# Kernel tuning notes

Measured on AMD Instinct MI355X. Metric: run time of the kernel, lower is better.

## Reference

```python
import jax, jax.numpy as jnp
import numpy as np
import math

ANSWER_LEN = 11; D_MODEL = 6; FFN_DIM = 3; HEAD_DIM = 3; MAX_SEQ_LEN = 34
N_HEADS = 2; POS_DIM = 3; TOK_DIM = 3; VOCAB_SIZE = 14; MAX_DIGITS = 10
EOS_TOKEN = 12; EQUALS_TOKEN = 11; PAD_TOKEN = 13; PLUS_TOKEN = 10
B, T = 65536, 34


def _spiral(i, period):
    return (math.cos(2 * math.pi * i / period), math.sin(2 * math.pi * i / period), i / max(period - 1, 1))


def _build_pos_enc():
    N_POS = 10
    pe = np.zeros((MAX_SEQ_LEN, POS_DIM), dtype=np.float32)
    for i in range(MAX_DIGITS):
        pe[i] = _spiral(i, N_POS)
    for i in range(MAX_DIGITS):
        pe[11 + i] = _spiral(i, N_POS)
    for i in range(min(ANSWER_LEN, N_POS)):
        pe[22 + i] = _spiral(i, N_POS)
    pe[32] = [0.0, 0.0, 1.5]
    pe[10] = [2.0, 0.0, -1.0]
    pe[21] = [0.0, 2.0, -1.0]
    pe[33] = [-2.0, 0.0, -1.0]
    return pe


def _build_tok_emb():
    emb = np.zeros((VOCAB_SIZE, TOK_DIM), dtype=np.float32)
    for d in range(10):
        emb[d] = _spiral(d, 10)
    emb[PLUS_TOKEN] = [2.0, 0.0, -1.0]
    emb[EQUALS_TOKEN] = [0.0, 2.0, -1.0]
    emb[EOS_TOKEN] = [-2.0, 0.0, -1.0]
    emb[PAD_TOKEN] = [0.0, -2.0, -1.0]
    return emb


def setup_inputs() -> dict:
    key = jax.random.key(0)
    ks = jax.random.split(key, 12)
    H = N_HEADS * HEAD_DIM  # 6

    def lin(k, out_d, in_d):
        bound = 1.0 / math.sqrt(in_d)
        return jax.random.uniform(k, (out_d, in_d), jnp.float32, -bound, bound)

    return {
        'idx': jax.random.randint(ks[0], (B, T), 0, VOCAB_SIZE),
        'tok_emb': jnp.asarray(_build_tok_emb()),
        'pos_enc': jnp.asarray(_build_pos_enc()),
        'q_w': lin(ks[1], H, POS_DIM),
        'k_w': lin(ks[2], H, POS_DIM),
        'v_w': lin(ks[3], H, TOK_DIM),
        'out_w': lin(ks[4], D_MODEL, H),
        'ln1_g': jnp.ones((D_MODEL,)), 'ln1_b': jnp.zeros((D_MODEL,)),
        'ln2_g': jnp.ones((D_MODEL,)), 'ln2_b': jnp.zeros((D_MODEL,)),
        'lnf_g': jnp.ones((D_MODEL,)), 'lnf_b': jnp.zeros((D_MODEL,)),
        'ffn_w1': lin(ks[5], FFN_DIM, D_MODEL),
        'ffn_b1': jax.random.uniform(ks[6], (FFN_DIM,), jnp.float32, -1/math.sqrt(D_MODEL), 1/math.sqrt(D_MODEL)),
        'ffn_w2': lin(ks[7], D_MODEL, FFN_DIM),
        'ffn_b2': jax.random.uniform(ks[8], (D_MODEL,), jnp.float32, -1/math.sqrt(FFN_DIM), 1/math.sqrt(FFN_DIM)),
        'head_w': lin(ks[9], TOK_DIM, D_MODEL),
    }


def _ln(x, g, b, eps=1e-5):
    mu = jnp.mean(x, -1, keepdims=True)
    var = jnp.mean((x - mu) ** 2, -1, keepdims=True)
    return (x - mu) * jax.lax.rsqrt(var + eps) * g + b


def reference(idx, tok_emb, pos_enc, q_w, k_w, v_w, out_w,
              ln1_g, ln1_b, ln2_g, ln2_b, lnf_g, lnf_b,
              ffn_w1, ffn_b1, ffn_w2, ffn_b2, head_w):
    b, t = idx.shape
    tok = tok_emb[idx]                              # [B,T,3]
    pos = jnp.broadcast_to(pos_enc[:t][None], (b, t, POS_DIM))
    x = jnp.concatenate([tok, pos], -1)             # [B,T,6]
    h = _ln(x, ln1_g, ln1_b)
    x_tok, x_pos = h[..., :TOK_DIM], h[..., TOK_DIM:]
    q = (x_pos @ q_w.T).reshape(b, t, N_HEADS, HEAD_DIM)
    k = (x_pos @ k_w.T).reshape(b, t, N_HEADS, HEAD_DIM)
    v = (x_tok @ v_w.T).reshape(b, t, N_HEADS, HEAD_DIM)
    attn = jnp.einsum('bqhd,bkhd->bhqk', q, k) / math.sqrt(HEAD_DIM)
    mask = jnp.tril(jnp.ones((t, t), dtype=bool))
    attn = jnp.where(mask[None, None], attn, -jnp.inf)
    attn = jax.nn.softmax(attn, -1)
    out = jnp.einsum('bhqk,bkhd->bqhd', attn, v).reshape(b, t, N_HEADS * HEAD_DIM)
    x = x + out @ out_w.T
    h2 = _ln(x, ln2_g, ln2_b)
    ffn = jax.nn.gelu(h2 @ ffn_w1.T + ffn_b1, approximate=False) @ ffn_w2.T + ffn_b2
    x = x + ffn
    x = _ln(x, lnf_g, lnf_b)
    return (x @ head_w.T) @ tok_emb.T               # [B,T,VOCAB]
```

## Files before the change

### kernel.cpp

```cpp
#include <hip/hip_runtime.h>
#include <math.h>

#define TT  34
#define VV  14
#define BLK 256


__global__ __launch_bounds__(BLK) void addtx_fwd(
    const int*   __restrict__ idx,
    const float* __restrict__ tok_emb,
    const float* __restrict__ pos_enc,
    const float* __restrict__ q_w,
    const float* __restrict__ k_w,
    const float* __restrict__ v_w,
    const float* __restrict__ out_w,
    const float* __restrict__ ln1_g, const float* __restrict__ ln1_b,
    const float* __restrict__ ln2_g, const float* __restrict__ ln2_b,
    const float* __restrict__ lnf_g, const float* __restrict__ lnf_b,
    const float* __restrict__ ffn_w1, const float* __restrict__ ffn_b1,
    const float* __restrict__ ffn_w2, const float* __restrict__ ffn_b2,
    const float* __restrict__ head_w,
    float* __restrict__ out)
{
    __shared__ float4 kvtab[TT * VV * 3];
    __shared__ float  wsm[192];
    __shared__ float  lgs[BLK * VV];

    const int tid = threadIdx.x;
    const int blk = blockIdx.x;

    {
        const int i = tid;
        if (i < 36)       wsm[i] = out_w[i];
        else if (i < 42)  wsm[i] = ln2_g[i - 36];
        else if (i < 48)  wsm[i] = ln2_b[i - 42];
        else if (i < 66)  wsm[i] = ffn_w1[i - 48];
        else if (i < 69)  wsm[i] = ffn_b1[i - 66];
        else if (i < 87)  wsm[i] = ffn_w2[i - 69];
        else if (i < 93)  wsm[i] = ffn_b2[i - 87];
        else if (i < 99)  wsm[i] = lnf_g[i - 93];
        else if (i < 105) wsm[i] = lnf_b[i - 99];
        else if (i < 189) {
            const int j = i - 105, v = j / 6, d = j - v * 6;
            wsm[i] = head_w[0 * 6 + d] * tok_emb[v * 3 + 0]
                   + head_w[1 * 6 + d] * tok_emb[v * 3 + 1]
                   + head_w[2 * 6 + d] * tok_emb[v * 3 + 2];
        }
    }

    const float rs3 = 0.57735026918962576f;
    for (int e = tid; e < TT * VV; e += BLK) {
        const int pos = e / VV, id = e - pos * VV;
        float x[6];
        x[0] = tok_emb[id * 3 + 0]; x[1] = tok_emb[id * 3 + 1]; x[2] = tok_emb[id * 3 + 2];
        x[3] = pos_enc[pos * 3 + 0]; x[4] = pos_enc[pos * 3 + 1]; x[5] = pos_enc[pos * 3 + 2];
        float mu = (x[0] + x[1] + x[2] + x[3] + x[4] + x[5]) * (1.0f / 6.0f);
        float var = 0.0f;
        #pragma unroll
        for (int d = 0; d < 6; ++d) { float dd = x[d] - mu; var += dd * dd; }
        const float rstd = rsqrtf(var * (1.0f / 6.0f) + 1e-5f);
        float h[6];
        #pragma unroll
        for (int d = 0; d < 6; ++d) h[d] = (x[d] - mu) * rstd * ln1_g[d] + ln1_b[d];
        float kk[6], vvv[6];
        #pragma unroll
        for (int r = 0; r < 6; ++r) {
            kk[r]  = (h[3] * k_w[r * 3 + 0] + h[4] * k_w[r * 3 + 1] + h[5] * k_w[r * 3 + 2]) * rs3;
            vvv[r] =  h[0] * v_w[r * 3 + 0] + h[1] * v_w[r * 3 + 1] + h[2] * v_w[r * 3 + 2];
        }
        kvtab[e * 3 + 0] = make_float4(kk[0], kk[1], kk[2], kk[3]);
        kvtab[e * 3 + 1] = make_float4(kk[4], kk[5], vvv[0], vvv[1]);
        kvtab[e * 3 + 2] = make_float4(vvv[2], vvv[3], vvv[4], vvv[5]);
    }
    __syncthreads();

    const int srank = (tid + ((blk & 3) << 6)) & (BLK - 1);
    const int r0 = (blk * BLK) % TT;
    int rem = srank, dsel = 0, ksel = 0, found = 0;
    #pragma unroll 1
    for (int tau = 0; tau < TT; ++tau) {
        int dlt = tau - r0; if (dlt < 0) dlt += TT;
        const int c = (dlt < (BLK % TT)) ? (BLK / TT + 1) : (BLK / TT);
        if (!found) {
            if (rem < c) { dsel = dlt; ksel = rem; found = 1; }
            else rem -= c;
        }
    }
    const int il   = dsel + ksel * TT;
    const int flat = blk * BLK + il;
    const int b    = flat / TT;
    const int t    = flat - b * TT;
    const int* __restrict__ row = idx + b * TT;

    float x[6];
    {
        const int mid = row[t];
        x[0] = tok_emb[mid * 3 + 0]; x[1] = tok_emb[mid * 3 + 1]; x[2] = tok_emb[mid * 3 + 2];
        x[3] = pos_enc[t * 3 + 0];   x[4] = pos_enc[t * 3 + 1];   x[5] = pos_enc[t * 3 + 2];
    }
    float q[6];
    {
        float mu = (x[0] + x[1] + x[2] + x[3] + x[4] + x[5]) * (1.0f / 6.0f);
        float var = 0.0f;
        #pragma unroll
        for (int d = 0; d < 6; ++d) { float dd = x[d] - mu; var += dd * dd; }
        const float rstd = rsqrtf(var * (1.0f / 6.0f) + 1e-5f);
        float h[6];
        #pragma unroll
        for (int d = 0; d < 6; ++d) h[d] = (x[d] - mu) * rstd * ln1_g[d] + ln1_b[d];
        #pragma unroll
        for (int r = 0; r < 6; ++r)
            q[r] = h[3] * q_w[r * 3 + 0] + h[4] * q_w[r * 3 + 1] + h[5] * q_w[r * 3 + 2];
    }

    float l0 = 0.f, l1 = 0.f;
    float a0 = 0.f, a1 = 0.f, a2 = 0.f, a3 = 0.f, a4 = 0.f, a5 = 0.f;
    int ebase = 0;
    for (int s = 0; s <= t; ++s) {
        const int ids = row[s];
        const float4* e4 = &kvtab[(ebase + ids) * 3];
        const float4 ka = e4[0];
        const float4 kb = e4[1];
        const float4 vb = e4[2];
        const float sc0 = q[0] * ka.x + q[1] * ka.y + q[2] * ka.z;
        const float sc1 = q[3] * ka.w + q[4] * kb.x + q[5] * kb.y;
        const float p0 = __expf(sc0);
        const float p1 = __expf(sc1);
        l0 += p0; l1 += p1;
        a0 += p0 * kb.z; a1 += p0 * kb.w; a2 += p0 * vb.x;
        a3 += p1 * vb.y; a4 += p1 * vb.z; a5 += p1 * vb.w;
        ebase += VV;
    }
    const float i0 = 1.0f / l0, i1 = 1.0f / l1;
    const float o6[6] = { a0 * i0, a1 * i0, a2 * i0, a3 * i1, a4 * i1, a5 * i1 };

    #pragma unroll
    for (int d = 0; d < 6; ++d) {
        float s = x[d];
        #pragma unroll
        for (int j = 0; j < 6; ++j) s += o6[j] * wsm[d * 6 + j];
        x[d] = s;
    }

    {
        float mu = (x[0] + x[1] + x[2] + x[3] + x[4] + x[5]) * (1.0f / 6.0f);
        float var = 0.0f;
        #pragma unroll
        for (int d = 0; d < 6; ++d) { float dd = x[d] - mu; var += dd * dd; }
        const float rstd = rsqrtf(var * (1.0f / 6.0f) + 1e-5f);
        float h2[6];
        #pragma unroll
        for (int d = 0; d < 6; ++d) h2[d] = (x[d] - mu) * rstd * wsm[36 + d] + wsm[42 + d];
        float g3[3];
        #pragma unroll
        for (int i = 0; i < 3; ++i) {
            float f = wsm[66 + i];
            #pragma unroll
            for (int d = 0; d < 6; ++d) f += h2[d] * wsm[48 + i * 6 + d];
            g3[i] = 0.5f * f * (1.0f + erff(f * 0.70710678118654752f));
        }
        #pragma unroll
        for (int d = 0; d < 6; ++d) {
            float s = x[d] + wsm[87 + d];
            #pragma unroll
            for (int i = 0; i < 3; ++i) s += g3[i] * wsm[69 + d * 3 + i];
            x[d] = s;
        }
    }

    {
        float mu = (x[0] + x[1] + x[2] + x[3] + x[4] + x[5]) * (1.0f / 6.0f);
        float var = 0.0f;
        #pragma unroll
        for (int d = 0; d < 6; ++d) { float dd = x[d] - mu; var += dd * dd; }
        const float rstd = rsqrtf(var * (1.0f / 6.0f) + 1e-5f);
        float xf[6];
        #pragma unroll
        for (int d = 0; d < 6; ++d) xf[d] = (x[d] - mu) * rstd * wsm[93 + d] + wsm[99 + d];
        #pragma unroll
        for (int v = 0; v < VV; ++v) {
            float s = 0.0f;
            #pragma unroll
            for (int d = 0; d < 6; ++d) s += xf[d] * wsm[105 + v * 6 + d];
            lgs[il * VV + v] = s;
        }
    }
    __syncthreads();

    float* __restrict__ ob = out + (size_t)blk * (BLK * VV);
    #pragma unroll
    for (int j = 0; j < VV; ++j)
        ob[j * BLK + tid] = lgs[j * BLK + tid];
}

extern "C" void kernel_launch(void* const* d_in, const int* in_sizes, int n_in,
                              void* d_out, int out_size, void* d_ws, size_t ws_size,
                              hipStream_t stream) {
    const int*   idx     = (const int*)  d_in[0];
    const float* tok_emb = (const float*)d_in[1];
    const float* pos_enc = (const float*)d_in[2];
    const float* q_w     = (const float*)d_in[3];
    const float* k_w     = (const float*)d_in[4];
    const float* v_w     = (const float*)d_in[5];
    const float* out_w   = (const float*)d_in[6];
    const float* ln1_g   = (const float*)d_in[7];
    const float* ln1_b   = (const float*)d_in[8];
    const float* ln2_g   = (const float*)d_in[9];
    const float* ln2_b   = (const float*)d_in[10];
    const float* lnf_g   = (const float*)d_in[11];
    const float* lnf_b   = (const float*)d_in[12];
    const float* ffn_w1  = (const float*)d_in[13];
    const float* ffn_b1  = (const float*)d_in[14];
    const float* ffn_w2  = (const float*)d_in[15];
    const float* ffn_b2  = (const float*)d_in[16];
    const float* head_w  = (const float*)d_in[17];
    float* out = (float*)d_out;

    const int n = in_sizes[0];
    const int blocks = n / BLK;
    addtx_fwd<<<blocks, BLK, 0, stream>>>(idx, tok_emb, pos_enc, q_w, k_w, v_w, out_w,
                                          ln1_g, ln1_b, ln2_g, ln2_b, lnf_g, lnf_b,
                                          ffn_w1, ffn_b1, ffn_w2, ffn_b2, head_w, out);
}
```

Baseline: 254.9 us.

## Stage token ids and embeddings in LDS, reuse KV table for output staging

```diff
diff --git a/kernel.cpp b/kernel.cpp
--- a/kernel.cpp
+++ b/kernel.cpp
@@ -4,6 +4,12 @@
 #define TT  34
 #define VV  14
 #define BLK 256
+
+#if __has_builtin(__builtin_amdgcn_exp2f)
+#define EXP2F(x) __builtin_amdgcn_exp2f(x)
+#else
+#define EXP2F(x) exp2f(x)
+#endif
 
 
 __global__ __launch_bounds__(BLK) void addtx_fwd(
@@ -22,9 +28,9 @@
     const float* __restrict__ head_w,
     float* __restrict__ out)
 {
-    __shared__ float4 kvtab[TT * VV * 3];
-    __shared__ float  wsm[192];
-    __shared__ float  lgs[BLK * VV];
+    __shared__ float4 kvs[TT * VV * 3];
+    __shared__ float  wsm[336];
+    __shared__ int    idsb[308];
 
     const int tid = threadIdx.x;
     const int blk = blockIdx.x;
@@ -46,9 +52,23 @@
                    + head_w[1 * 6 + d] * tok_emb[v * 3 + 1]
                    + head_w[2 * 6 + d] * tok_emb[v * 3 + 2];
         }
-    }
-
-    const float rs3 = 0.57735026918962576f;
+        if (tid < 144) {
+            const int k2 = 192 + tid;
+            wsm[k2] = (k2 < 234) ? tok_emb[k2 - 192] : pos_enc[k2 - 234];
+        }
+    }
+
+    const int ntot = (int)gridDim.x * BLK;
+    const int b0   = (blk * BLK) / TT;
+    {
+        const int gb = b0 * TT;
+        for (int e = tid; e < 308; e += BLK) {
+            const int g = gb + e;
+            idsb[e] = (g < ntot) ? idx[g] : 0;
+        }
+    }
+
+    const float rs3l = 0.57735026918962576f * 1.4426950408889634f;
     for (int e = tid; e < TT * VV; e += BLK) {
         const int pos = e / VV, id = e - pos * VV;
         float x[6];
@@ -65,38 +85,41 @@
         float kk[6], vvv[6];
         #pragma unroll
         for (int r = 0; r < 6; ++r) {
-            kk[r]  = (h[3] * k_w[r * 3 + 0] + h[4] * k_w[r * 3 + 1] + h[5] * k_w[r * 3 + 2]) * rs3;
+            kk[r]  = (h[3] * k_w[r * 3 + 0] + h[4] * k_w[r * 3 + 1] + h[5] * k_w[r * 3 + 2]) * rs3l;
             vvv[r] =  h[0] * v_w[r * 3 + 0] + h[1] * v_w[r * 3 + 1] + h[2] * v_w[r * 3 + 2];
         }
-        kvtab[e * 3 + 0] = make_float4(kk[0], kk[1], kk[2], kk[3]);
-        kvtab[e * 3 + 1] = make_float4(kk[4], kk[5], vvv[0], vvv[1]);
-        kvtab[e * 3 + 2] = make_float4(vvv[2], vvv[3], vvv[4], vvv[5]);
+        kvs[e * 3 + 0] = make_float4(kk[0], kk[1], kk[2], kk[3]);
+        kvs[e * 3 + 1] = make_float4(kk[4], kk[5], vvv[0], vvv[1]);
+        kvs[e * 3 + 2] = make_float4(vvv[2], vvv[3], vvv[4], vvv[5]);
     }
     __syncthreads();
 
     const int srank = (tid + ((blk & 3) << 6)) & (BLK - 1);
     const int r0 = (blk * BLK) % TT;
-    int rem = srank, dsel = 0, ksel = 0, found = 0;
-    #pragma unroll 1
-    for (int tau = 0; tau < TT; ++tau) {
-        int dlt = tau - r0; if (dlt < 0) dlt += TT;
-        const int c = (dlt < (BLK % TT)) ? (BLK / TT + 1) : (BLK / TT);
-        if (!found) {
-            if (rem < c) { dsel = dlt; ksel = rem; found = 1; }
-            else rem -= c;
-        }
+    const int m  = (TT - r0) % TT;
+    int dsel, ksel;
+    if (m < 18) {
+        const int nA = (18 - m) << 3;
+        if (srank < nA)            { dsel = m + (srank >> 3); ksel = srank & 7; }
+        else if (srank < nA + 112) { const int r = srank - nA;       dsel = 18 + r / 7; ksel = r % 7; }
+        else                       { const int r = srank - nA - 112; dsel = r >> 3;     ksel = r & 7; }
+    } else {
+        const int nA = (TT - m) * 7;
+        if (srank < nA)            { dsel = m + srank / 7; ksel = srank % 7; }
+        else if (srank < nA + 144) { const int r = srank - nA;       dsel = r >> 3;     ksel = r & 7; }
+        else                       { const int r = srank - nA - 144; dsel = 18 + r / 7; ksel = r % 7; }
     }
     const int il   = dsel + ksel * TT;
     const int flat = blk * BLK + il;
     const int b    = flat / TT;
     const int t    = flat - b * TT;
-    const int* __restrict__ row = idx + b * TT;
+    const int* __restrict__ rowL = idsb + (b - b0) * TT;
 
     float x[6];
     {
-        const int mid = row[t];
-        x[0] = tok_emb[mid * 3 + 0]; x[1] = tok_emb[mid * 3 + 1]; x[2] = tok_emb[mid * 3 + 2];
-        x[3] = pos_enc[t * 3 + 0];   x[4] = pos_enc[t * 3 + 1];   x[5] = pos_enc[t * 3 + 2];
+        const int mid = rowL[t];
+        x[0] = wsm[192 + mid * 3]; x[1] = wsm[193 + mid * 3]; x[2] = wsm[194 + mid * 3];
+        x[3] = wsm[234 + t * 3];   x[4] = wsm[235 + t * 3];   x[5] = wsm[236 + t * 3];
     }
     float q[6];
     {
@@ -115,21 +138,22 @@
 
     float l0 = 0.f, l1 = 0.f;
     float a0 = 0.f, a1 = 0.f, a2 = 0.f, a3 = 0.f, a4 = 0.f, a5 = 0.f;
-    int ebase = 0;
+    int ids = rowL[0];
+    int sb = 0;
     for (int s = 0; s <= t; ++s) {
-        const int ids = row[s];
-        const float4* e4 = &kvtab[(ebase + ids) * 3];
+        const float4* e4 = kvs + (sb + ids * 3);
         const float4 ka = e4[0];
         const float4 kb = e4[1];
         const float4 vb = e4[2];
+        ids = rowL[s + 1];
         const float sc0 = q[0] * ka.x + q[1] * ka.y + q[2] * ka.z;
         const float sc1 = q[3] * ka.w + q[4] * kb.x + q[5] * kb.y;
-        const float p0 = __expf(sc0);
-        const float p1 = __expf(sc1);
+        const float p0 = EXP2F(sc0);
+        const float p1 = EXP2F(sc1);
         l0 += p0; l1 += p1;
         a0 += p0 * kb.z; a1 += p0 * kb.w; a2 += p0 * vb.x;
         a3 += p1 * vb.y; a4 += p1 * vb.z; a5 += p1 * vb.w;
-        ebase += VV;
+        sb += VV * 3;
     }
     const float i0 = 1.0f / l0, i1 = 1.0f / l1;
     const float o6[6] = { a0 * i0, a1 * i0, a2 * i0, a3 * i1, a4 * i1, a5 * i1 };
@@ -168,6 +192,7 @@
         }
     }
 
+    float lg[VV];
     {
         float mu = (x[0] + x[1] + x[2] + x[3] + x[4] + x[5]) * (1.0f / 6.0f);
         float var = 0.0f;
@@ -182,15 +207,21 @@
             float s = 0.0f;
             #pragma unroll
             for (int d = 0; d < 6; ++d) s += xf[d] * wsm[105 + v * 6 + d];
-            lgs[il * VV + v] = s;
-        }
-    }
+            lg[v] = s;
+        }
+    }
+
     __syncthreads();
-
-    float* __restrict__ ob = out + (size_t)blk * (BLK * VV);
+    float2* lg2 = reinterpret_cast<float2*>(kvs);
     #pragma unroll
-    for (int j = 0; j < VV; ++j)
-        ob[j * BLK + tid] = lgs[j * BLK + tid];
+    for (int j = 0; j < 7; ++j)
+        lg2[il * 7 + j] = make_float2(lg[2 * j], lg[2 * j + 1]);
+    __syncthreads();
+    const float2* s2 = reinterpret_cast<const float2*>(kvs);
+    float2* __restrict__ ob2 = reinterpret_cast<float2*>(out + (size_t)blk * (BLK * VV));
+    #pragma unroll
+    for (int j = 0; j < 7; ++j)
+        ob2[j * BLK + tid] = s2[j * BLK + tid];
 }
 
 extern "C" void kernel_launch(void* const* d_in, const int* in_sizes, int n_in,
```

Measured after the change: 222.8 us. 12.6% less time.
